# Kernel optimization log

Hardware: AMD Instinct MI355X
Metric: run time of the kernel (lower is better)

The kernel has to match this reference:

```python
import jax, jax.numpy as jnp
import numpy as np

L, E, H, S, V, F = 8, 1024, 16, 2048, 32000, 4096
NEG = -1e9  # mask value used by the original (triu * -1e9)


def setup_inputs() -> dict:
    key = jax.random.key(0)
    ks = jax.random.split(key, 10)
    s = 0.02  # init scale to keep activations stable without residuals/LN
    return {
        "inpt": jax.random.randint(ks[0], (S,), 0, V, dtype=jnp.int32),
        "num_heads": H,
        "emb_table": jax.random.normal(ks[1], (V, E), dtype=jnp.float32) * s,
        "Wq": jax.random.normal(ks[2], (L, E, E), dtype=jnp.float32) * s,
        "bq": jnp.zeros((L, E), dtype=jnp.float32),
        "Wk": jax.random.normal(ks[3], (L, E, E), dtype=jnp.float32) * s,
        "bk": jnp.zeros((L, E), dtype=jnp.float32),
        "Wv": jax.random.normal(ks[4], (L, E, E), dtype=jnp.float32) * s,
        "bv": jnp.zeros((L, E), dtype=jnp.float32),
        "W1": jax.random.normal(ks[5], (L, E, F), dtype=jnp.float32) * s,
        "b1": jnp.zeros((L, F), dtype=jnp.float32),
        "W2": jax.random.normal(ks[6], (L, F, E), dtype=jnp.float32) * s,
        "b2": jnp.zeros((L, E), dtype=jnp.float32),
        "Wout": jax.random.normal(ks[7], (E, V), dtype=jnp.float32) * s,
    }


def reference(inpt, num_heads, emb_table, Wq, bq, Wk, bk, Wv, bv, W1, b1, W2, b2, Wout):
    x = emb_table[inpt]                      # [S, E] embedding lookup
    seq_len, emb_dim = x.shape
    head_dim = emb_dim // num_heads
    scale = head_dim ** 0.5
    n_layers = Wq.shape[0]
    # additive causal mask, exactly as torch.triu(ones)*-1e9
    mask = jnp.triu(jnp.full((seq_len, seq_len), NEG, dtype=x.dtype), k=1)

    for l in range(n_layers):  # fixed small layer count
        q = (x @ Wq[l] + bq[l]).reshape(seq_len, num_heads, head_dim).transpose(1, 0, 2)
        k = (x @ Wk[l] + bk[l]).reshape(seq_len, num_heads, head_dim).transpose(1, 0, 2)
        v = (x @ Wv[l] + bv[l]).reshape(seq_len, num_heads, head_dim).transpose(1, 0, 2)
        scores = jnp.einsum('hqd,hkd->hqk', q, k) / scale + mask  # [H, S, S]
        probs = jax.nn.softmax(scores, axis=-1)
        attn = jnp.einsum('hqk,hkd->hqd', probs, v)               # [H, S, D]
        attn = attn.transpose(1, 0, 2).reshape(seq_len, emb_dim)  # [S, E]
        # NOTE: original has no residual connection; x is replaced by FFN(attn)
        x = jax.nn.relu(attn @ W1[l] + b1[l]) @ W2[l] + b2[l]

    return x @ Wout  # [S, V] logits (no bias, no softmax in original forward)
```

## Files before the change

### kernel.cpp

```cpp
#include <hip/hip_runtime.h>
#include <hip/hip_fp16.h>


#define SS 2048
#define EE 1024
#define NH 16
#define FF 4096
#define NV 32000
#define NL 8

typedef _Float16 f16;
typedef _Float16 f16x8 __attribute__((ext_vector_type(8)));
typedef _Float16 f16x4 __attribute__((ext_vector_type(4)));
typedef float f32x4 __attribute__((ext_vector_type(4)));

#define CS 4096.0f
#define INV_CS 0.000244140625f
#define SCORE_SCALE 7.450580596923828e-09f
#define SCORE_SCALE2 1.0748631e-08f

__device__ __forceinline__ void gload16(const void* g, void* lds) {
    __builtin_amdgcn_global_load_lds(
        (const __attribute__((address_space(1))) unsigned int*)g,
        (__attribute__((address_space(3))) unsigned int*)lds, 16, 0, 0);
}

#define BAR do { asm volatile("" ::: "memory"); __builtin_amdgcn_s_barrier(); } while (0)

__global__ void k_embed(const int* __restrict__ ids, const float* __restrict__ emb,
                        f16* __restrict__ xh) {
    int s = blockIdx.x;
    int e = threadIdx.x * 4;
    const float4 v = *(const float4*)&emb[(size_t)ids[s] * EE + e];
    f16x4 h;
    h[0] = (f16)(v.x * CS); h[1] = (f16)(v.y * CS);
    h[2] = (f16)(v.z * CS); h[3] = (f16)(v.w * CS);
    *(f16x4*)&xh[(size_t)s * EE + e] = h;
}

__device__ __forceinline__ void tr64(const float* __restrict__ in, f16* __restrict__ out,
                                     int ldi, int ldo, int bx, int by) {
    __shared__ float tl[64][65];
    const int tx = threadIdx.x & 15, ty = threadIdx.x >> 4;
#pragma unroll
    for (int i = 0; i < 4; i++) {
        float4 v = *(const float4*)&in[(size_t)(by + ty * 4 + i) * ldi + bx + tx * 4];
        tl[ty * 4 + i][tx * 4 + 0] = v.x;
        tl[ty * 4 + i][tx * 4 + 1] = v.y;
        tl[ty * 4 + i][tx * 4 + 2] = v.z;
        tl[ty * 4 + i][tx * 4 + 3] = v.w;
    }
    __syncthreads();
#pragma unroll
    for (int i = 0; i < 4; i++) {
        f16x4 h;
#pragma unroll
        for (int j = 0; j < 4; j++) h[j] = (f16)tl[tx * 4 + j][ty * 4 + i];
        *(f16x4*)&out[(size_t)(bx + ty * 4 + i) * ldo + by + tx * 4] = h;
    }
}

__global__ void k_trW(const float* __restrict__ Wq, const float* __restrict__ Wk,
                      const float* __restrict__ Wv, const float* __restrict__ W1,
                      const float* __restrict__ W2,
                      const float* __restrict__ bq, const float* __restrict__ bk,
                      const float* __restrict__ bv,
                      f16* __restrict__ wqkvt, f16* __restrict__ w1t,
                      f16* __restrict__ w2t, float* __restrict__ bqkv) {
    int b = blockIdx.x;
    if (b == 2816) {
        int i = threadIdx.x;
#pragma unroll
        for (int j = 0; j < 12; j++) {
            int idx = j * 256 + i;
            bqkv[idx] = idx < EE ? bq[idx] : (idx < 2 * EE ? bk[idx - EE] : bv[idx - 2 * EE]);
        }
        return;
    }
    if (b < 768) {
        int s = b >> 8, t2 = b & 255;
        tr64(s == 0 ? Wq : (s == 1 ? Wk : Wv), wqkvt + (size_t)s * EE * EE,
             EE, EE, (t2 & 15) * 64, (t2 >> 4) * 64);
    } else if (b < 1792) {
        int t2 = b - 768;
        tr64(W1, w1t, FF, EE, (t2 & 63) * 64, (t2 >> 6) * 64);
    } else {
        int t2 = b - 1792;
        tr64(W2, w2t, EE, FF, (t2 & 15) * 64, (t2 >> 4) * 64);
    }
}

__global__ void k_trOut(const float* __restrict__ in, f16* __restrict__ out) {
    int b = blockIdx.x;
    tr64(in, out, NV, EE, (b % 500) * 64, (b / 500) * 64);
}

__global__ void k_combine4(const float* __restrict__ part, const float* __restrict__ bias,
                           f16* __restrict__ out) {
    const size_t sz = (size_t)SS * EE;
    int i = (blockIdx.x * 256 + threadIdx.x) * 4;
    float4 a = *(const float4*)&part[i];
    float4 b = *(const float4*)&part[i + sz];
    float4 c = *(const float4*)&part[i + 2 * sz];
    float4 d = *(const float4*)&part[i + 3 * sz];
    float4 bb = *(const float4*)&bias[i & (EE - 1)];
    f16x4 h;
    h[0] = (f16)(a.x + b.x + c.x + d.x + bb.x * CS);
    h[1] = (f16)(a.y + b.y + c.y + d.y + bb.y * CS);
    h[2] = (f16)(a.z + b.z + c.z + d.z + bb.z * CS);
    h[3] = (f16)(a.w + b.w + c.w + d.w + bb.w * CS);
    *(f16x4*)&out[i] = h;
}

template<int BM, int BN, int TAG>
__global__ __launch_bounds__((BM == 128) ? 256 : 512, 2) void k_gemm(
    const f16* __restrict__ A, const f16* __restrict__ B,
    const float* __restrict__ bias, f16* __restrict__ Ch, float* __restrict__ Cf,
    f16* __restrict__ VtOut,
    int M, int N, int Kstride, int Ksub, int nm, int nn, int kch,
    float bscale, float oscale, int relu) {
    constexpr int WR = (BM == 256) ? ((BN == 256) ? 2 : 4) : 2;
    constexpr int WC = (BN == 256) ? 4 : 2;
    constexpr int NW = WR * WC;
    constexpr int THREADS = NW * 64;
    constexpr int MR = BM / WR / 16;
    constexpr int RPC = THREADS / 8;
    constexpr int ACALLS = BM / RPC;
    constexpr int BCALLS = BN / RPC;
    constexpr int LPT = ACALLS + BCALLS;

    __shared__ f16 As[2][BM * 64];
    __shared__ f16 Bs[2][BN * 64];

    const int t = threadIdx.x;
    const int l = t & 63, w = t >> 6;
    const int lr = l & 15, lc = l >> 4;

    const int nwg = nm * nn * kch;
    const int q8 = nwg >> 3, r8 = nwg & 7;
    const int xcd = blockIdx.x & 7, lid = blockIdx.x >> 3;
    const int wgid = (xcd < r8 ? xcd * (q8 + 1) : r8 * (q8 + 1) + (xcd - r8) * q8) + lid;
    const int kc = wgid / (nm * nn);
    const int rem = wgid - kc * (nm * nn);
    const int m0 = (rem % nm) * BM, n0 = (rem / nm) * BN;

    const f16* Ab = A + (size_t)kc * Ksub;
    const f16* Bb = B + (size_t)kc * Ksub;
    float* Cfb = Cf ? Cf + (size_t)kc * M * N : nullptr;

    const int wr = w / WC, wc = w % WC;

    f32x4 acc[MR][4] = {};

    const int srow = t >> 3;
    const int scol = 8 * ((t & 7) ^ (srow & 7));
    const int NT = Ksub / 64;

#define STAGE(bb, tt_) { \
    const size_t kof = (size_t)(tt_) * 64 + scol; \
    _Pragma("unroll") \
    for (int c = 0; c < ACALLS; c++) \
        gload16(Ab + (size_t)(m0 + c * RPC + srow) * Kstride + kof, \
                (char*)As[bb] + c * (RPC * 128) + w * 1024); \
    _Pragma("unroll") \
    for (int c = 0; c < BCALLS; c++) \
        gload16(Bb + (size_t)(n0 + c * RPC + srow) * Kstride + kof, \
                (char*)Bs[bb] + c * (RPC * 128) + w * 1024); }

    STAGE(0, 0)
    STAGE(1, 1)
    asm volatile("s_waitcnt vmcnt(%0)" :: "n"(LPT) : "memory");
    BAR;

    int cur = 0;
    for (int tt = 0; tt < NT; ++tt) {
        const f16* pA = As[cur];
        const f16* pB = Bs[cur];
#pragma unroll
        for (int ks = 0; ks < 2; ks++) {
            f16x8 af[MR], bf[4];
#pragma unroll
            for (int m = 0; m < MR; m++) {
                const int row = wr * (MR * 16) + m * 16 + lr;
                af[m] = *(const f16x8*)&pA[row * 64 + 8 * ((ks * 4 + lc) ^ (row & 7))];
            }
#pragma unroll
            for (int n = 0; n < 4; n++) {
                const int row = wc * 64 + n * 16 + lr;
                bf[n] = *(const f16x8*)&pB[row * 64 + 8 * ((ks * 4 + lc) ^ (row & 7))];
            }
            __builtin_amdgcn_s_setprio(1);
#pragma unroll
            for (int m = 0; m < MR; m++)
#pragma unroll
                for (int n = 0; n < 4; n++)
                    acc[m][n] = __builtin_amdgcn_mfma_f32_16x16x32_f16(af[m], bf[n], acc[m][n], 0, 0, 0);
            __builtin_amdgcn_s_setprio(0);
        }
        BAR;
        if (tt + 2 < NT) {
            STAGE(cur, tt + 2)
            asm volatile("s_waitcnt vmcnt(%0)" :: "n"(LPT) : "memory");
        } else if (tt + 1 < NT) {
            asm volatile("s_waitcnt vmcnt(0)" ::: "memory");
        }
        BAR;
        cur ^= 1;
    }
#undef STAGE

#pragma unroll
    for (int m = 0; m < MR; m++)
#pragma unroll
        for (int n = 0; n < 4; n++) {
            const int row0 = m0 + wr * (MR * 16) + m * 16 + lc * 4;
            const int col = n0 + wc * 64 + n * 16 + lr;
            float v[4];
#pragma unroll
            for (int r = 0; r < 4; r++) {
                v[r] = acc[m][n][r];
                if (bias) v[r] += bias[col] * bscale;
                if (relu) v[r] = fmaxf(v[r], 0.0f);
            }
            if (VtOut && col >= 2 * EE) {
                f16x4 h4;
#pragma unroll
                for (int r = 0; r < 4; r++) h4[r] = (f16)v[r];
                *(f16x4*)&VtOut[(size_t)(col - 2 * EE) * SS + row0] = h4;
            } else if (Ch) {
#pragma unroll
                for (int r = 0; r < 4; r++)
                    Ch[(size_t)(row0 + r) * N + col] = (f16)v[r];
            } else {
#pragma unroll
                for (int r = 0; r < 4; r++)
                    Cfb[(size_t)(row0 + r) * N + col] = v[r] * oscale;
            }
        }
}

__global__ __launch_bounds__(512, 2) void k_gemm4p(
    const f16* __restrict__ A, const f16* __restrict__ B, float* __restrict__ Cf,
    int N, int K, int nm, int nn, float oscale) {
    __shared__ f16 As[2][256 * 64];
    __shared__ f16 Bs[2][256 * 64];
    const int t = threadIdx.x;
    const int l = t & 63, w = t >> 6;
    const int lr = l & 15, lc = l >> 4;

    const int nwg = nm * nn;
    const int q8 = nwg >> 3, r8 = nwg & 7;
    const int xcd = blockIdx.x & 7, lid = blockIdx.x >> 3;
    const int wgid = (xcd < r8 ? xcd * (q8 + 1) : r8 * (q8 + 1) + (xcd - r8) * q8) + lid;
    const int m0 = (wgid % nm) * 256, n0 = (wgid / nm) * 256;

    const int wr = w >> 2, wc = w & 3;

    f32x4 acc[8][4] = {};
    f16x8 aF[2][4], bF[2][4];

    const int srow = t >> 3;
    const int scol = 8 * ((t & 7) ^ (srow & 7));
    const int NT = K / 64;

#define SG_A(bb, tt_, c) \
    gload16(A + (size_t)(m0 + (c) * 64 + srow) * K + (size_t)(tt_) * 64 + scol, \
            (char*)As[bb] + (c) * 8192 + w * 1024);
#define SG_B(bb, tt_, c) \
    gload16(B + (size_t)(n0 + (c) * 64 + srow) * K + (size_t)(tt_) * 64 + scol, \
            (char*)Bs[bb] + (c) * 8192 + w * 1024);

#define LDA_HALF(pA_, mh) { _Pragma("unroll") \
    for (int ks = 0; ks < 2; ks++) _Pragma("unroll") \
    for (int m = 0; m < 4; m++) { \
        const int row = wr * 128 + ((mh) * 4 + m) * 16 + lr; \
        aF[ks][m] = *(const f16x8*)&pA_[row * 64 + 8 * ((ks * 4 + lc) ^ (row & 7))]; } }

#define LDB_PAIR(pB_, nb) { _Pragma("unroll") \
    for (int ks = 0; ks < 2; ks++) _Pragma("unroll") \
    for (int j = 0; j < 2; j++) { \
        const int row = wc * 64 + ((nb) + j) * 16 + lr; \
        bF[ks][(nb) + j] = *(const f16x8*)&pB_[row * 64 + 8 * ((ks * 4 + lc) ^ (row & 7))]; } }

#define PH_MMA(mb, nb) { __builtin_amdgcn_s_setprio(1); \
    _Pragma("unroll") for (int ks = 0; ks < 2; ks++) \
    _Pragma("unroll") for (int m = 0; m < 4; m++) \
    _Pragma("unroll") for (int j = 0; j < 2; j++) \
        acc[(mb) + m][(nb) + j] = __builtin_amdgcn_mfma_f32_16x16x32_f16( \
            aF[ks][m], bF[ks][(nb) + j], acc[(mb) + m][(nb) + j], 0, 0, 0); \
    __builtin_amdgcn_s_setprio(0); }

#pragma unroll
    for (int c = 0; c < 4; c++) { SG_A(0, 0, c) SG_B(0, 0, c) }
#pragma unroll
    for (int c = 0; c < 4; c++) { SG_A(1, 1, c) SG_B(1, 1, c) }
    asm volatile("s_waitcnt vmcnt(8)" ::: "memory");
    BAR;

    int cur = 0;
    for (int tt = 0; tt < NT; ++tt) {
        const f16* pA = As[cur];
        const f16* pB = Bs[cur];
        const bool pre = (tt + 2 < NT);

        LDA_HALF(pA, 0)
        LDB_PAIR(pB, 0)
        BAR;
        PH_MMA(0, 0)
        BAR;

        LDB_PAIR(pB, 2)
        if (pre) { SG_A(cur, tt + 2, 0) SG_A(cur, tt + 2, 2) }
        BAR;
        PH_MMA(0, 2)
        BAR;

        LDA_HALF(pA, 1)
        if (pre) { SG_B(cur, tt + 2, 0) SG_B(cur, tt + 2, 1)
                   SG_B(cur, tt + 2, 2) SG_B(cur, tt + 2, 3) }
        BAR;
        PH_MMA(4, 0)
        BAR;

        if (pre) {
            SG_A(cur, tt + 2, 1) SG_A(cur, tt + 2, 3)
            asm volatile("s_waitcnt vmcnt(8)" ::: "memory");
        } else if (tt + 1 < NT) {
            asm volatile("s_waitcnt vmcnt(0)" ::: "memory");
        }
        BAR;
        PH_MMA(4, 2)
        BAR;

        cur ^= 1;
    }
#undef SG_A
#undef SG_B
#undef LDA_HALF
#undef LDB_PAIR
#undef PH_MMA

#pragma unroll
    for (int m = 0; m < 8; m++)
#pragma unroll
        for (int n = 0; n < 4; n++) {
            const int row0 = m0 + wr * 128 + m * 16 + lc * 4;
            const int col = n0 + wc * 64 + n * 16 + lr;
#pragma unroll
            for (int r = 0; r < 4; r++)
                Cf[(size_t)(row0 + r) * N + col] = acc[m][n][r] * oscale;
        }
}

__global__ __launch_bounds__(256) void k_flash(
    const f16* __restrict__ qkv, const f16* __restrict__ vt, f16* __restrict__ attn) {
    __shared__ f16 Ks[2][128 * 64];
    __shared__ f16 Vs[2][64 * 128];
    __shared__ f16 Ps[4 * 16 * 128];
    const int h = blockIdx.x;
    const int y = blockIdx.y;
    const int qb = (y < 16) ? (31 - 2 * y) : (2 * (y - 16));
    const int t = threadIdx.x, l = t & 63, w = t >> 6;
    const int lr = l & 15, lc = l >> 4;
    const int q0 = qb * 64;
    const int qrow = q0 + w * 16 + lr;

    f16x8 qf0 = *(const f16x8*)&qkv[(size_t)qrow * 3072 + h * 64 + lc * 8];
    f16x8 qf1 = *(const f16x8*)&qkv[(size_t)qrow * 3072 + h * 64 + 32 + lc * 8];

    f32x4 o[4] = {};
    float mrun[4], lrun[4];
#pragma unroll
    for (int r = 0; r < 4; r++) { mrun[r] = -__builtin_inff(); lrun[r] = 0.0f; }

    const int krow = t >> 3;
    const int kscol = 8 * ((t & 7) ^ (krow & 7));
    const int vrow = t >> 4;
    const int vscol = 8 * ((t & 15) ^ (vrow & 7));
    const f16* gK = qkv + EE + h * 64;
    const f16* gV = vt + (size_t)(h * 64) * SS;
    f16* Pw = &Ps[w * 16 * 128];
    const int psw = (lr & 7) << 4;

#define FSTAGE(bb, kt_) { \
    _Pragma("unroll") \
    for (int c = 0; c < 4; c++) { \
        gload16(gK + (size_t)((kt_) * 128 + c * 32 + krow) * 3072 + kscol, \
                (char*)Ks[bb] + c * 4096 + w * 1024); \
        gload16(gV + (size_t)(c * 16 + vrow) * SS + (kt_) * 128 + vscol, \
                (char*)Vs[bb] + c * 4096 + w * 1024); } }

    const int nkt = (qb >> 1) + 1;
    FSTAGE(0, 0)
    FSTAGE(1, 1)
    asm volatile("s_waitcnt vmcnt(8)" ::: "memory");
    __builtin_amdgcn_s_barrier();

    int cur = 0;
    for (int kt = 0; kt < nkt; kt++) {
        f32x4 sc[8];
        __builtin_amdgcn_s_setprio(1);
#pragma unroll
        for (int kj = 0; kj < 8; kj++) {
            const int krw = kj * 16 + lr;
            const int sw = krw & 7;
            f16x8 kb0 = *(const f16x8*)&Ks[cur][krw * 64 + 8 * (lc ^ sw)];
            f16x8 kb1 = *(const f16x8*)&Ks[cur][krw * 64 + 8 * ((lc + 4) ^ sw)];
            f32x4 z = {};
            z = __builtin_amdgcn_mfma_f32_16x16x32_f16(qf0, kb0, z, 0, 0, 0);
            z = __builtin_amdgcn_mfma_f32_16x16x32_f16(qf1, kb1, z, 0, 0, 0);
            sc[kj] = z;
        }
        __builtin_amdgcn_s_setprio(0);

        const bool diag = (kt == nkt - 1);
#pragma unroll
        for (int kj = 0; kj < 8; kj++)
#pragma unroll
            for (int r = 0; r < 4; r++) {
                float v = sc[kj][r] * SCORE_SCALE2;
                if (diag) {
                    int kk = kt * 128 + kj * 16 + lr;
                    int qq = q0 + w * 16 + lc * 4 + r;
                    if (kk > qq) v = -__builtin_inff();
                }
                sc[kj][r] = v;
            }

        float mt[4];
#pragma unroll
        for (int r = 0; r < 4; r++) {
            float m2 = fmaxf(fmaxf(fmaxf(sc[0][r], sc[1][r]), fmaxf(sc[2][r], sc[3][r])),
                             fmaxf(fmaxf(sc[4][r], sc[5][r]), fmaxf(sc[6][r], sc[7][r])));
            m2 = fmaxf(m2, __shfl_xor(m2, 1));
            m2 = fmaxf(m2, __shfl_xor(m2, 2));
            m2 = fmaxf(m2, __shfl_xor(m2, 4));
            m2 = fmaxf(m2, __shfl_xor(m2, 8));
            mt[r] = m2;
        }
        bool need = (mt[0] > mrun[0] + 11.0f) || (mt[1] > mrun[1] + 11.0f) ||
                    (mt[2] > mrun[2] + 11.0f) || (mt[3] > mrun[3] + 11.0f);
        if (__any(need)) {
#pragma unroll
            for (int r = 0; r < 4; r++) {
                float mnew = fmaxf(mrun[r], mt[r]);
                float alpha = exp2f(mrun[r] - mnew);
                lrun[r] *= alpha;
                mrun[r] = mnew;
#pragma unroll
                for (int dj = 0; dj < 4; dj++) o[dj][r] *= alpha;
            }
        }
#pragma unroll
        for (int r = 0; r < 4; r++) {
            float psum = 0.0f;
#pragma unroll
            for (int kj = 0; kj < 8; kj++) {
                float p = exp2f(sc[kj][r] - mrun[r]);
                sc[kj][r] = p;
                psum += p;
            }
            psum += __shfl_xor(psum, 1);
            psum += __shfl_xor(psum, 2);
            psum += __shfl_xor(psum, 4);
            psum += __shfl_xor(psum, 8);
            lrun[r] += psum;
        }

#pragma unroll
        for (int kj = 0; kj < 8; kj++)
#pragma unroll
            for (int r = 0; r < 4; r++) {
                int prow = lc * 4 + r;
                int pb = prow * 256 + (((kj * 16 + lr) * 2) ^ ((prow & 7) << 4));
                *(f16*)((char*)Pw + pb) = (f16)sc[kj][r];
            }

        __builtin_amdgcn_s_setprio(1);
#pragma unroll
        for (int s2 = 0; s2 < 4; s2++) {
            f16x8 pa = *(const f16x8*)((const char*)Pw + lr * 256 + (((lc + 4 * s2) * 16) ^ psw));
#pragma unroll
            for (int dj = 0; dj < 4; dj++) {
                const int vr = dj * 16 + lr;
                f16x8 vb = *(const f16x8*)&Vs[cur][vr * 128 + 8 * ((s2 * 4 + lc) ^ (vr & 7))];
                o[dj] = __builtin_amdgcn_mfma_f32_16x16x32_f16(pa, vb, o[dj], 0, 0, 0);
            }
        }
        __builtin_amdgcn_s_setprio(0);

        asm volatile("" ::: "memory");
        __builtin_amdgcn_s_barrier();
        if (kt + 2 < nkt) {
            FSTAGE(cur, kt + 2)
            asm volatile("s_waitcnt vmcnt(8)" ::: "memory");
        } else if (kt + 1 < nkt) {
            asm volatile("s_waitcnt vmcnt(0)" ::: "memory");
        }
        __builtin_amdgcn_s_barrier();
        cur ^= 1;
    }
#undef FSTAGE

#pragma unroll
    for (int dj = 0; dj < 4; dj++)
#pragma unroll
        for (int r = 0; r < 4; r++) {
            float v = o[dj][r] / lrun[r];
            attn[(size_t)(q0 + w * 16 + lc * 4 + r) * EE + h * 64 + dj * 16 + lr] = (f16)v;
        }
}

extern "C" void kernel_launch(void* const* d_in, const int* in_sizes, int n_in,
                              void* d_out, int out_size, void* d_ws, size_t ws_size,
                              hipStream_t stream) {
    const int*   ids  = (const int*)d_in[0];
    const float* emb  = (const float*)d_in[2];
    const float* Wq   = (const float*)d_in[3];
    const float* bq   = (const float*)d_in[4];
    const float* Wk   = (const float*)d_in[5];
    const float* bk   = (const float*)d_in[6];
    const float* Wv   = (const float*)d_in[7];
    const float* bv   = (const float*)d_in[8];
    const float* W1   = (const float*)d_in[9];
    const float* b1   = (const float*)d_in[10];
    const float* W2   = (const float*)d_in[11];
    const float* b2   = (const float*)d_in[12];
    const float* Wout = (const float*)d_in[13];
    float* out = (float*)d_out;

    char* p = (char*)d_ws;
    f16* xh    = (f16*)p; p += (size_t)SS * EE * 2;
    f16* qkvh  = (f16*)p; p += (size_t)SS * 3 * EE * 2;
    f16* vt    = (f16*)p; p += (size_t)EE * SS * 2;
    f16* attn  = (f16*)p; p += (size_t)SS * EE * 2;
    f16* h1    = (f16*)p; p += (size_t)SS * FF * 2;
    f16* wqkvt = (f16*)p; p += (size_t)3 * EE * EE * 2;
    f16* w1t   = (f16*)p; p += (size_t)FF * EE * 2;
    f16* w2t   = (f16*)p; p += (size_t)EE * FF * 2;
    f16* woutt = (f16*)p; p += (size_t)NV * EE * 2;
    float* part = (float*)p; p += (size_t)4 * SS * EE * 4;
    float* bqkv = (float*)p; p += 3 * EE * 4;

    k_embed<<<SS, 256, 0, stream>>>(ids, emb, xh);

    for (int l = 0; l < NL; l++) {
        k_trW<<<2817, 256, 0, stream>>>(
            Wq + (size_t)l * EE * EE, Wk + (size_t)l * EE * EE, Wv + (size_t)l * EE * EE,
            W1 + (size_t)l * EE * FF, W2 + (size_t)l * FF * EE,
            bq + l * EE, bk + l * EE, bv + l * EE,
            wqkvt, w1t, w2t, bqkv);

        k_gemm<256, 128, 1><<<8 * 24, 512, 0, stream>>>(
            xh, wqkvt, bqkv, qkvh, nullptr, vt, SS, 3 * EE, EE, EE, 8, 24, 1, CS, 1.0f, 0);

        k_flash<<<dim3(NH, SS / 64), 256, 0, stream>>>(qkvh, vt, attn);

        k_gemm<256, 128, 2><<<8 * 32, 512, 0, stream>>>(
            attn, w1t, b1 + (size_t)l * FF, h1, nullptr, nullptr, SS, FF, EE, EE, 8, 32, 1, CS, 1.0f, 1);

        k_gemm<256, 128, 3><<<8 * 8 * 4, 512, 0, stream>>>(
            h1, w2t, nullptr, nullptr, part, nullptr, SS, EE, FF, FF / 4, 8, 8, 4, 0.0f, 1.0f, 0);
        k_combine4<<<SS * EE / 1024, 256, 0, stream>>>(part, b2 + (size_t)l * EE, xh);
    }

    k_trOut<<<8000, 256, 0, stream>>>(Wout, woutt);
    k_gemm4p<<<8 * 125, 512, 0, stream>>>(xh, woutt, out, NV, EE, 8, 125, INV_CS);
}
```

Measured before the change: 1.440 ms.

## Split GEMM main loop into four phases interleaving LDS reads, MFMA and prefetch

Replaces the templated GEMM with a fixed 256x128 variant whose K-tile loop runs in four phases. Each phase loads a pair of A/B fragments from LDS, issues a subset of MFMAs, and spreads the next tile's global-to-LDS loads across phases instead of issuing them all at once. The warp-to-output mapping becomes interleaved: rows strided by 64, columns by 32. This aims to overlap memory traffic with matrix math, at the cost of more barriers per K-tile.

```diff
diff --git a/kernel.cpp b/kernel.cpp
--- a/kernel.cpp
+++ b/kernel.cpp
@@ -16,7 +16,6 @@
 
 #define CS 4096.0f
 #define INV_CS 0.000244140625f
-#define SCORE_SCALE 7.450580596923828e-09f
 #define SCORE_SCALE2 1.0748631e-08f
 
 __device__ __forceinline__ void gload16(const void* g, void* lds) {
@@ -112,25 +111,15 @@
     *(f16x4*)&out[i] = h;
 }
 
-template<int BM, int BN, int TAG>
-__global__ __launch_bounds__((BM == 128) ? 256 : 512, 2) void k_gemm(
+template<int TAG>
+__global__ __launch_bounds__(512, 2) void k_g4p(
     const f16* __restrict__ A, const f16* __restrict__ B,
     const float* __restrict__ bias, f16* __restrict__ Ch, float* __restrict__ Cf,
     f16* __restrict__ VtOut,
     int M, int N, int Kstride, int Ksub, int nm, int nn, int kch,
     float bscale, float oscale, int relu) {
-    constexpr int WR = (BM == 256) ? ((BN == 256) ? 2 : 4) : 2;
-    constexpr int WC = (BN == 256) ? 4 : 2;
-    constexpr int NW = WR * WC;
-    constexpr int THREADS = NW * 64;
-    constexpr int MR = BM / WR / 16;
-    constexpr int RPC = THREADS / 8;
-    constexpr int ACALLS = BM / RPC;
-    constexpr int BCALLS = BN / RPC;
-    constexpr int LPT = ACALLS + BCALLS;
-
-    __shared__ f16 As[2][BM * 64];
-    __shared__ f16 Bs[2][BN * 64];
+    __shared__ f16 As[2][256 * 64];
+    __shared__ f16 Bs[2][128 * 64];
 
     const int t = threadIdx.x;
     const int l = t & 63, w = t >> 6;
@@ -142,79 +131,105 @@
     const int wgid = (xcd < r8 ? xcd * (q8 + 1) : r8 * (q8 + 1) + (xcd - r8) * q8) + lid;
     const int kc = wgid / (nm * nn);
     const int rem = wgid - kc * (nm * nn);
-    const int m0 = (rem % nm) * BM, n0 = (rem / nm) * BN;
+    const int m0 = (rem % nm) * 256, n0 = (rem / nm) * 128;
 
     const f16* Ab = A + (size_t)kc * Ksub;
     const f16* Bb = B + (size_t)kc * Ksub;
     float* Cfb = Cf ? Cf + (size_t)kc * M * N : nullptr;
 
-    const int wr = w / WC, wc = w % WC;
-
-    f32x4 acc[MR][4] = {};
+    const int wr = w >> 1, wc = w & 1;
+
+    f32x4 acc[4][4] = {};
+    f16x8 aF[2][2], bF[2][4];
 
     const int srow = t >> 3;
     const int scol = 8 * ((t & 7) ^ (srow & 7));
     const int NT = Ksub / 64;
 
-#define STAGE(bb, tt_) { \
-    const size_t kof = (size_t)(tt_) * 64 + scol; \
-    _Pragma("unroll") \
-    for (int c = 0; c < ACALLS; c++) \
-        gload16(Ab + (size_t)(m0 + c * RPC + srow) * Kstride + kof, \
-                (char*)As[bb] + c * (RPC * 128) + w * 1024); \
-    _Pragma("unroll") \
-    for (int c = 0; c < BCALLS; c++) \
-        gload16(Bb + (size_t)(n0 + c * RPC + srow) * Kstride + kof, \
-                (char*)Bs[bb] + c * (RPC * 128) + w * 1024); }
-
-    STAGE(0, 0)
-    STAGE(1, 1)
-    asm volatile("s_waitcnt vmcnt(%0)" :: "n"(LPT) : "memory");
+#define SG_A(bb, tt_, c) \
+    gload16(Ab + (size_t)(m0 + (c) * 64 + srow) * Kstride + (size_t)(tt_) * 64 + scol, \
+            (char*)As[bb] + (c) * 8192 + w * 1024);
+#define SG_B(bb, tt_, c) \
+    gload16(Bb + (size_t)(n0 + (c) * 64 + srow) * Kstride + (size_t)(tt_) * 64 + scol, \
+            (char*)Bs[bb] + (c) * 8192 + w * 1024);
+
+#define LDA_PAIR(pA_, mh) { _Pragma("unroll") \
+    for (int ks = 0; ks < 2; ks++) _Pragma("unroll") \
+    for (int j = 0; j < 2; j++) { \
+        const int row = ((mh) * 2 + j) * 64 + wr * 16 + lr; \
+        aF[ks][j] = *(const f16x8*)&pA_[row * 64 + 8 * ((ks * 4 + lc) ^ (row & 7))]; } }
+
+#define LDB_PAIR(pB_, nb) { _Pragma("unroll") \
+    for (int ks = 0; ks < 2; ks++) _Pragma("unroll") \
+    for (int j = 0; j < 2; j++) { \
+        const int row = ((nb) + j) * 32 + wc * 16 + lr; \
+        bF[ks][(nb) + j] = *(const f16x8*)&pB_[row * 64 + 8 * ((ks * 4 + lc) ^ (row & 7))]; } }
+
+#define PH_MMA(mb, nb) { __builtin_amdgcn_s_setprio(1); \
+    _Pragma("unroll") for (int ks = 0; ks < 2; ks++) \
+    _Pragma("unroll") for (int j = 0; j < 2; j++) \
+    _Pragma("unroll") for (int n = 0; n < 2; n++) \
+        acc[(mb) + j][(nb) + n] = __builtin_amdgcn_mfma_f32_16x16x32_f16( \
+            aF[ks][j], bF[ks][(nb) + n], acc[(mb) + j][(nb) + n], 0, 0, 0); \
+    __builtin_amdgcn_s_setprio(0); }
+
+#pragma unroll
+    for (int c = 0; c < 4; c++) { SG_A(0, 0, c) }
+    SG_B(0, 0, 0) SG_B(0, 0, 1)
+#pragma unroll
+    for (int c = 0; c < 4; c++) { SG_A(1, 1, c) }
+    SG_B(1, 1, 0) SG_B(1, 1, 1)
+    asm volatile("s_waitcnt vmcnt(6)" ::: "memory");
     BAR;
 
     int cur = 0;
     for (int tt = 0; tt < NT; ++tt) {
         const f16* pA = As[cur];
         const f16* pB = Bs[cur];
-#pragma unroll
-        for (int ks = 0; ks < 2; ks++) {
-            f16x8 af[MR], bf[4];
-#pragma unroll
-            for (int m = 0; m < MR; m++) {
-                const int row = wr * (MR * 16) + m * 16 + lr;
-                af[m] = *(const f16x8*)&pA[row * 64 + 8 * ((ks * 4 + lc) ^ (row & 7))];
-            }
-#pragma unroll
-            for (int n = 0; n < 4; n++) {
-                const int row = wc * 64 + n * 16 + lr;
-                bf[n] = *(const f16x8*)&pB[row * 64 + 8 * ((ks * 4 + lc) ^ (row & 7))];
-            }
-            __builtin_amdgcn_s_setprio(1);
-#pragma unroll
-            for (int m = 0; m < MR; m++)
-#pragma unroll
-                for (int n = 0; n < 4; n++)
-                    acc[m][n] = __builtin_amdgcn_mfma_f32_16x16x32_f16(af[m], bf[n], acc[m][n], 0, 0, 0);
-            __builtin_amdgcn_s_setprio(0);
-        }
-        BAR;
-        if (tt + 2 < NT) {
-            STAGE(cur, tt + 2)
-            asm volatile("s_waitcnt vmcnt(%0)" :: "n"(LPT) : "memory");
+        const bool pre = (tt + 2 < NT);
+
+        LDA_PAIR(pA, 0)
+        LDB_PAIR(pB, 0)
+        BAR;
+        PH_MMA(0, 0)
+        BAR;
+
+        LDB_PAIR(pB, 2)
+        if (pre) { SG_A(cur, tt + 2, 0) SG_A(cur, tt + 2, 1) SG_B(cur, tt + 2, 0) }
+        BAR;
+        PH_MMA(0, 2)
+        BAR;
+
+        LDA_PAIR(pA, 1)
+        if (pre) { SG_B(cur, tt + 2, 1) }
+        BAR;
+        PH_MMA(2, 0)
+        BAR;
+
+        if (pre) {
+            SG_A(cur, tt + 2, 2) SG_A(cur, tt + 2, 3)
+            asm volatile("s_waitcnt vmcnt(6)" ::: "memory");
         } else if (tt + 1 < NT) {
             asm volatile("s_waitcnt vmcnt(0)" ::: "memory");
         }
         BAR;
+        PH_MMA(2, 2)
+        BAR;
+
         cur ^= 1;
     }
-#undef STAGE
-
-#pragma unroll
-    for (int m = 0; m < MR; m++)
+#undef SG_A
+#undef SG_B
+#undef LDA_PAIR
+#undef LDB_PAIR
+#undef PH_MMA
+
+#pragma unroll
+    for (int m = 0; m < 4; m++)
 #pragma unroll
         for (int n = 0; n < 4; n++) {
-            const int row0 = m0 + wr * (MR * 16) + m * 16 + lc * 4;
-            const int col = n0 + wc * 64 + n * 16 + lr;
+            const int row0 = m0 + m * 64 + wr * 16 + lc * 4;
+            const int col = n0 + n * 32 + wc * 16 + lr;
             float v[4];
 #pragma unroll
             for (int r = 0; r < 4; r++) {
@@ -551,15 +566,15 @@
             bq + l * EE, bk + l * EE, bv + l * EE,
             wqkvt, w1t, w2t, bqkv);
 
-        k_gemm<256, 128, 1><<<8 * 24, 512, 0, stream>>>(
+        k_g4p<1><<<8 * 24, 512, 0, stream>>>(
             xh, wqkvt, bqkv, qkvh, nullptr, vt, SS, 3 * EE, EE, EE, 8, 24, 1, CS, 1.0f, 0);
 
         k_flash<<<dim3(NH, SS / 64), 256, 0, stream>>>(qkvh, vt, attn);
 
-        k_gemm<256, 128, 2><<<8 * 32, 512, 0, stream>>>(
+        k_g4p<2><<<8 * 32, 512, 0, stream>>>(
             attn, w1t, b1 + (size_t)l * FF, h1, nullptr, nullptr, SS, FF, EE, EE, 8, 32, 1, CS, 1.0f, 1);
 
-        k_gemm<256, 128, 3><<<8 * 8 * 4, 512, 0, stream>>>(
+        k_g4p<3><<<8 * 8 * 4, 512, 0, stream>>>(
             h1, w2t, nullptr, nullptr, part, nullptr, SS, EE, FF, FF / 4, 8, 8, 4, 0.0f, 1.0f, 0);
         k_combine4<<<SS * EE / 1024, 256, 0, stream>>>(part, b2 + (size_t)l * EE, xh);
     }
```

New measurement: 1.479 ms. 1.03x slower.
